# Optimization experiments

Measured on AMD Instinct MI355X. Metric: run time of the kernel, lower is better.

Reference implementation:

```python
import jax, jax.numpy as jnp
import numpy as np

B, C, RES, WS, HEADS, GROUPS, MLP_DIM = 16, 256, 56, 7, 8, 16, 1024
HEAD_DIM = C // HEADS
N = WS * WS  # tokens per window


def _rel_index(ws):
    coords = np.stack(np.meshgrid(np.arange(ws), np.arange(ws), indexing='ij'), 0).reshape(2, -1)
    rel = (coords[:, :, None] - coords[:, None, :]).transpose(1, 2, 0) + ws - 1
    return jnp.asarray(rel[..., 0] * (2 * ws - 1) + rel[..., 1], jnp.int32)


def setup_inputs() -> dict:
    key = jax.random.key(0)
    ks = jax.random.split(key, 8)
    s = 0.02
    return {
        'x': jax.random.normal(ks[0], (B, C, RES, RES), jnp.float32),
        'qkv_w': jax.random.normal(ks[1], (3 * C, C), jnp.float32) * s,
        'qkv_b': jnp.zeros((3 * C,), jnp.float32),
        'logit_scale': jnp.full((HEADS,), np.log(10.0), jnp.float32),
        'bias_table': jax.random.normal(ks[2], ((2 * WS - 1) ** 2, HEADS), jnp.float32) * s,
        'rel_index': _rel_index(WS),
        'proj_w': jax.random.normal(ks[3], (C, C), jnp.float32) * s,
        'proj_b': jnp.zeros((C,), jnp.float32),
        'gn1_w': jnp.ones((C,), jnp.float32), 'gn1_b': jnp.zeros((C,), jnp.float32),
        'gn2_w': jnp.ones((C,), jnp.float32), 'gn2_b': jnp.zeros((C,), jnp.float32),
        'mlp_gn_w': jnp.ones((C,), jnp.float32), 'mlp_gn_b': jnp.zeros((C,), jnp.float32),
        'mlp_w1': jax.random.normal(ks[4], (MLP_DIM, C), jnp.float32) * s,
        'mlp_b1': jnp.zeros((MLP_DIM,), jnp.float32),
        'mlp_w2': jax.random.normal(ks[5], (C, MLP_DIM), jnp.float32) * s,
        'mlp_b2': jnp.zeros((C,), jnp.float32),
    }


def _group_norm(x, w, b, groups, eps=1e-5):
    bn, c, h, ww = x.shape
    xg = x.reshape(bn, groups, c // groups, h, ww)
    m = xg.mean((2, 3, 4), keepdims=True)
    v = xg.var((2, 3, 4), keepdims=True)
    xg = (xg - m) * jax.lax.rsqrt(v + eps)
    return xg.reshape(bn, c, h, ww) * w[None, :, None, None] + b[None, :, None, None]


def _window_cosine_attn(x, qkv_w, qkv_b, logit_scale, bias_table, rel_index, proj_w, proj_b):
    bn, c, hh, ww = x.shape
    nh, nw = hh // WS, ww // WS
    # partition into non-overlapping WSxWS windows -> [bn*nh*nw, N, C]
    xw = x.reshape(bn, c, nh, WS, nw, WS).transpose(0, 2, 4, 3, 5, 1).reshape(bn * nh * nw, N, c)
    qkv = xw @ qkv_w.T + qkv_b
    qkv = qkv.reshape(-1, N, 3, HEADS, HEAD_DIM).transpose(2, 0, 3, 1, 4)
    q, k, v = qkv[0], qkv[1], qkv[2]  # [Bw, heads, N, d]
    # cosine attention (Swin v2): l2-normalized q/k, learnable clamped logit scale
    qn = q / jnp.clip(jnp.linalg.norm(q, axis=-1, keepdims=True), 1e-12)
    kn = k / jnp.clip(jnp.linalg.norm(k, axis=-1, keepdims=True), 1e-12)
    scale = jnp.exp(jnp.minimum(logit_scale, jnp.log(100.0)))[None, :, None, None]
    attn = jnp.einsum('bhnd,bhmd->bhnm', qn, kn) * scale
    bias = bias_table[rel_index].transpose(2, 0, 1)  # [heads, N, N]
    attn = jax.nn.softmax(attn + bias[None], axis=-1)
    out = jnp.einsum('bhnm,bhmd->bhnd', attn, v)
    out = out.transpose(0, 2, 1, 3).reshape(-1, N, c) @ proj_w.T + proj_b
    # reverse window partition -> [bn, c, H, W]
    out = out.reshape(bn, nh, nw, WS, WS, c).transpose(0, 5, 1, 3, 2, 4).reshape(bn, c, hh, ww)
    return out


def reference(x, qkv_w, qkv_b, logit_scale, bias_table, rel_index, proj_w, proj_b,
              gn1_w, gn1_b, gn2_w, gn2_b, mlp_gn_w, mlp_gn_b, mlp_w1, mlp_b1, mlp_w2, mlp_b2):
    h = _window_cosine_attn(x, qkv_w, qkv_b, logit_scale, bias_table, rel_index, proj_w, proj_b)
    h = jax.nn.relu(_group_norm(x + h, gn1_w, gn1_b, GROUPS))
    # ConvMLP: GroupNorm -> 1x1 conv -> act -> 1x1 conv
    m = _group_norm(h, mlp_gn_w, mlp_gn_b, GROUPS)
    m = jax.nn.relu(jnp.einsum('bchw,ec->behw', m, mlp_w1) + mlp_b1[None, :, None, None])
    m = jnp.einsum('behw,ce->bchw', m, mlp_w2) + mlp_b2[None, :, None, None]
    z = jax.nn.relu(_group_norm(h + m, gn2_w, gn2_b, GROUPS))
    return z
```

## Files before the change

kernel.cpp:

```cpp
#include <hip/hip_runtime.h>
#include <hip/hip_bf16.h>

typedef unsigned short u16;
typedef u16 u16x8 __attribute__((ext_vector_type(8)));
typedef u16 u16x4 __attribute__((ext_vector_type(4)));
typedef __bf16 bf16x8 __attribute__((ext_vector_type(8)));
typedef float f32x4 __attribute__((ext_vector_type(4)));

#define B_      16
#define C_      256
#define RES_    56
#define HW_     3136
#define NTOK    49
#define HEADS_  8
#define HD_     32
#define GROUPS_ 16
#define MLPD    1024
#define M_TOT   50176

__device__ __forceinline__ float b2f(u16 u){
  unsigned int x = ((unsigned int)u) << 16;
  return __builtin_bit_cast(float, x);
}
__device__ __forceinline__ u16 f2b(float f){
  __hip_bfloat16 h = __float2bfloat16(f);
  return __builtin_bit_cast(u16, h);
}
__device__ __forceinline__ bool sniff_f32(const void* sniff){
  return ((const u16*)sniff)[0] != (u16)0x3F80;
}
__device__ __forceinline__ float ldf(const void* p, size_t i, bool f32){
  return f32 ? ((const float*)p)[i] : b2f(((const u16*)p)[i]);
}
__device__ __forceinline__ void load8(const void* p, size_t off, bool f32, float* v){
  if (f32){
    const float* s = (const float*)p + off;
    float4 a = *(const float4*)s, b = *(const float4*)(s + 4);
    v[0]=a.x; v[1]=a.y; v[2]=a.z; v[3]=a.w; v[4]=b.x; v[5]=b.y; v[6]=b.z; v[7]=b.w;
  } else {
    u16x8 u = *(const u16x8*)((const u16*)p + off);
    #pragma unroll
    for (int j=0;j<8;++j) v[j] = b2f(u[j]);
  }
}

__device__ __forceinline__ void gload16(const u16* g, u16* l){
  __builtin_amdgcn_global_load_lds(
      (const __attribute__((address_space(1))) unsigned int*)g,
      (__attribute__((address_space(3))) unsigned int*)l, 16, 0, 0);
}

__device__ __forceinline__ int tok_of(int base_hw, int i){
  int ic = i < 48 ? i : 48;
  int q = (ic*37) >> 8;
  return base_hw + q*RES_ + (ic - q*7);
}

enum { M_QKV=0, M_PROJ=1, M_MLP1=2, M_MLP2=3 };

template<int MODE>
__global__ __launch_bounds__(256)
void mgemm(const u16* __restrict__ A, const u16* __restrict__ Bseg,
           const void* __restrict__ bias, void* __restrict__ Cp,
           const void* __restrict__ resid, const void* __restrict__ sniff)
{
  constexpr int KK = (MODE==M_MLP2) ? 1024 : 256;
  const int nx  = gridDim.x;
  const int bid = blockIdx.y * nx + blockIdx.x;
  const int cpx = (nx * gridDim.y) >> 3;
  const int swz = (bid & 7) * cpx + (bid >> 3);
  const int n0 = (swz % nx) * 128;
  const int m0 = (swz / nx) * 128;

  __shared__ alignas(16) u16 As[128*64];
  __shared__ alignas(16) u16 Bs[128*64];
  const int tid  = threadIdx.x;
  const int lane = tid & 63, w = tid >> 6;
  const int wm = w >> 1, wn = w & 1;
  const int lr = lane & 15, lk = lane >> 4;

  const int grow = lane >> 3, gcolg = (lane & 7) ^ (lane >> 3);
  size_t aoff[4], boff[4];
  #pragma unroll
  for (int i=0;i<4;++i){
    const int row = w*32 + i*8 + grow;
    aoff[i] = (size_t)(m0 + row)*KK + gcolg*8;
    boff[i] = (size_t)(n0 + row)*KK + gcolg*8;
  }

  f32x4 acc[4][4];
  #pragma unroll
  for (int i=0;i<4;++i)
    #pragma unroll
    for (int j=0;j<4;++j) acc[i][j] = (f32x4){0.f,0.f,0.f,0.f};

  for (int k0 = 0; k0 < KK; k0 += 64){
    if (k0) __syncthreads();
    #pragma unroll
    for (int i=0;i<4;++i){
      gload16(A    + aoff[i] + k0, As + (w*4+i)*512);
      gload16(Bseg + boff[i] + k0, Bs + (w*4+i)*512);
    }
    __syncthreads();
    #pragma unroll
    for (int kh=0; kh<2; ++kh){
      bf16x8 af[4], bfr[4];
      #pragma unroll
      for (int mf=0;mf<4;++mf){
        int row = wm*64 + mf*16 + lr;
        int idx = (row*64 + (kh*4 + lk)*8) ^ ((row&7)*8);
        af[mf] = *(const bf16x8*)(As + idx);
      }
      #pragma unroll
      for (int nf=0;nf<4;++nf){
        int row = wn*64 + nf*16 + lr;
        int idx = (row*64 + (kh*4 + lk)*8) ^ ((row&7)*8);
        bfr[nf] = *(const bf16x8*)(Bs + idx);
      }
      #pragma unroll
      for (int mf=0;mf<4;++mf)
        #pragma unroll
        for (int nf=0;nf<4;++nf)
          acc[mf][nf] = __builtin_amdgcn_mfma_f32_16x16x32_bf16(af[mf], bfr[nf], acc[mf][nf], 0,0,0);
    }
  }

  const bool f32 = sniff_f32(sniff);
  float bv[4];
  #pragma unroll
  for (int nf=0;nf<4;++nf) bv[nf] = ldf(bias, (size_t)(n0 + wn*64 + nf*16 + lr), f32);

  #pragma unroll
  for (int mf=0;mf<4;++mf){
    #pragma unroll
    for (int r=0;r<4;++r){
      const int row = m0 + wm*64 + mf*16 + lk*4 + r;
      #pragma unroll
      for (int nf=0;nf<4;++nf){
        const int col = n0 + wn*64 + nf*16 + lr;
        float v = acc[mf][nf][r] + bv[nf];
        if (MODE == M_QKV){
          ((u16*)Cp)[(size_t)row*768 + col] = f2b(v);
        } else if (MODE == M_PROJ){
          v += b2f(((const u16*)resid)[(size_t)row*C_ + col]);
          ((float*)Cp)[(size_t)row*C_ + col] = v;
        } else if (MODE == M_MLP1){
          ((u16*)Cp)[(size_t)row*MLPD + col] = f2b(fmaxf(v, 0.f));
        } else {
          v += ((const float*)resid)[(size_t)row*C_ + col];
          ((float*)Cp)[(size_t)row*C_ + col] = v;
        }
      }
    }
  }
}

__global__ __launch_bounds__(256)
void xt_kernel(const void* __restrict__ x, u16* __restrict__ xbf,
               const void* __restrict__ sniff){
  const bool f32 = sniff_f32(sniff);
  const int hw0 = blockIdx.x*64, c0 = blockIdx.y*64, b = blockIdx.z;
  __shared__ float tile[64][65];
  const int t = threadIdx.x;
  {
    int r = t >> 2, p = t & 3;
    size_t src = ((size_t)(b*C_ + c0 + r))*HW_ + hw0 + p*16;
    float v[16];
    load8(x, src, f32, v);
    load8(x, src + 8, f32, v + 8);
    #pragma unroll
    for (int e=0;e<16;++e) tile[p*16+e][r] = v[e];
  }
  __syncthreads();
  {
    int r2 = t >> 2, p2 = t & 3;
    u16x8 o0, o1;
    #pragma unroll
    for (int e=0;e<8;++e){ o0[e] = f2b(tile[r2][p2*16+e]); o1[e] = f2b(tile[r2][p2*16+8+e]); }
    size_t dst = ((size_t)(b*HW_ + hw0 + r2))*C_ + c0 + p2*16;
    *(u16x8*)(xbf + dst)     = o0;
    *(u16x8*)(xbf + dst + 8) = o1;
  }
}

__global__ __launch_bounds__(256)
void wconv(const void* __restrict__ src, u16* __restrict__ dst, int n,
           const void* __restrict__ sniff){
  const bool f32 = sniff_f32(sniff);
  int i = (blockIdx.x*256 + threadIdx.x)*8;
  if (i >= n) return;
  float v[8];
  load8(src, (size_t)i, f32, v);
  u16x8 u;
  #pragma unroll
  for (int j=0;j<8;++j) u[j] = f2b(v[j]);
  *(u16x8*)(dst + i) = u;
}

__global__ __launch_bounds__(256)
void bias_pre(const void* __restrict__ bias_table, const int* __restrict__ rel_index,
              float* __restrict__ out, float* __restrict__ rmax,
              const void* __restrict__ sniff){
  const bool f32 = sniff_f32(sniff);
  int h = blockIdx.x;
  for (int idx = threadIdx.x; idx < NTOK*NTOK; idx += 256)
    out[h*NTOK*NTOK + idx] = ldf(bias_table, (size_t)rel_index[idx]*HEADS_ + h, f32);
  __syncthreads();
  for (int i = threadIdx.x; i < NTOK; i += 256){
    const float* row = out + (h*NTOK + i)*NTOK;
    float m = row[0];
    for (int j=1;j<NTOK;++j) m = fmaxf(m, row[j]);
    rmax[h*NTOK + i] = m;
  }
}

__global__ __launch_bounds__(256)
void attn_kernel(const u16* __restrict__ qkv, u16* __restrict__ attnout,
                 const void* __restrict__ logit_scale, const float* __restrict__ biasD,
                 const float* __restrict__ biasRM, const void* __restrict__ sniff)
{
  const bool f32 = sniff_f32(sniff);
  const int h = blockIdx.x & 7, w = blockIdx.x >> 3;
  const int b = w >> 6, wr = (w >> 3) & 7, wc = w & 7;
  const int tid = threadIdx.x;
  const int wv = tid >> 6, lane = tid & 63;
  const int lr = lane & 15, lg = lane >> 4;
  const int base_hw = (wr*7)*RES_ + wc*7;
  const size_t qbase = (size_t)b*HW_*768;

  __shared__ alignas(16) u16 Qn[64][40];
  __shared__ alignas(16) u16 Kn[64][40];
  __shared__ alignas(16) u16 Vt[32][72];
  __shared__ alignas(16) u16 Pl[64][72];

  const float scale = __expf(fminf(ldf(logit_scale, h, f32), 4.6051701860f));

  if (wv == 0){
    u16 vrow[32];
    if (lane < NTOK){
      const u16* src = qkv + qbase + (size_t)tok_of(base_hw, lane)*768 + 512 + h*HD_;
      u16x8 a0 = *(const u16x8*)(src), a1 = *(const u16x8*)(src+8);
      u16x8 a2 = *(const u16x8*)(src+16), a3 = *(const u16x8*)(src+24);
      #pragma unroll
      for (int e=0;e<8;++e){ vrow[e]=a0[e]; vrow[8+e]=a1[e]; vrow[16+e]=a2[e]; vrow[24+e]=a3[e]; }
    } else {
      #pragma unroll
      for (int e=0;e<32;++e) vrow[e] = 0;
    }
    #pragma unroll
    for (int d=0;d<32;++d) Vt[d][lane] = vrow[d];
  } else if (wv == 1 || wv == 2){
    float fv[32];
    if (lane < NTOK){
      const u16* src = qkv + qbase + (size_t)tok_of(base_hw, lane)*768
                     + (wv == 2 ? 0 : 256) + h*HD_;
      #pragma unroll
      for (int c8=0;c8<4;++c8){
        u16x8 u = *(const u16x8*)(src + c8*8);
        #pragma unroll
        for (int e=0;e<8;++e) fv[c8*8+e] = b2f(u[e]);
      }
    } else {
      #pragma unroll
      for (int e=0;e<32;++e) fv[e] = 0.f;
    }
    float ss = 0.f;
    #pragma unroll
    for (int d=0;d<32;++d) ss += fv[d]*fv[d];
    float inv = (wv == 2 ? scale : 1.f) / fmaxf(sqrtf(ss), 1e-12f);
    u16* dst = (wv == 2) ? &Qn[lane][0] : &Kn[lane][0];
    #pragma unroll
    for (int c8=0;c8<4;++c8){
      u16x8 u;
      #pragma unroll
      for (int e=0;e<8;++e) u[e] = f2b(fv[c8*8+e]*inv);
      *(u16x8*)(dst + c8*8) = u;
    }
  }
  __syncthreads();

  const int mt = wv;
  const int i0 = mt*16;

  bf16x8 af = *(const bf16x8*)&Qn[i0 + lr][lg*8];
  f32x4 s[4];
  #pragma unroll
  for (int nt=0;nt<4;++nt){
    bf16x8 bq = *(const bf16x8*)&Kn[nt*16 + lr][lg*8];
    f32x4 c;
    #pragma unroll
    for (int r=0;r<4;++r){
      int i = i0 + lg*4 + r; if (i > 48) i = 48;
      int j = nt*16 + lr;    if (j > 48) j = 48;
      c[r] = biasD[((size_t)h*NTOK + i)*NTOK + j];
    }
    s[nt] = __builtin_amdgcn_mfma_f32_16x16x32_bf16(af, bq, c, 0,0,0);
  }

  float isum[4];
  #pragma unroll
  for (int r=0;r<4;++r){
    const int i = i0 + lg*4 + r;
    const int ic = i > 48 ? 48 : i;
    const float m = scale + biasRM[h*NTOK + ic];
    float ps = 0.f;
    #pragma unroll
    for (int nt=0;nt<4;++nt){
      const int j = nt*16 + lr;
      float p = (j < NTOK) ? __expf(s[nt][r] - m) : 0.f;
      Pl[i][j] = f2b(p);
      ps += p;
    }
    ps += __shfl_xor(ps,1); ps += __shfl_xor(ps,2);
    ps += __shfl_xor(ps,4); ps += __shfl_xor(ps,8);
    isum[r] = 1.f / ps;
  }

  f32x4 o[2];
  o[0] = (f32x4){0.f,0.f,0.f,0.f};
  o[1] = (f32x4){0.f,0.f,0.f,0.f};
  #pragma unroll
  for (int kk=0;kk<2;++kk){
    bf16x8 pa = *(const bf16x8*)&Pl[i0 + lr][kk*32 + lg*8];
    #pragma unroll
    for (int nt=0;nt<2;++nt){
      bf16x8 pb = *(const bf16x8*)&Vt[nt*16 + lr][kk*32 + lg*8];
      o[nt] = __builtin_amdgcn_mfma_f32_16x16x32_bf16(pa, pb, o[nt], 0,0,0);
    }
  }

  #pragma unroll
  for (int r=0;r<4;++r){
    const int i = i0 + lg*4 + r;
    if (i < NTOK){
      size_t ob = ((size_t)(b*HW_) + tok_of(base_hw, i))*C_ + h*HD_;
      attnout[ob + lr]      = f2b(o[0][r] * isum[r]);
      attnout[ob + 16 + lr] = f2b(o[1][r] * isum[r]);
    }
  }
}

__global__ __launch_bounds__(256)
void stats_part(const float* __restrict__ buf, float2* __restrict__ part){
  int chunk = blockIdx.x & 7;
  int g = (blockIdx.x >> 3) & 15;
  int b = blockIdx.x >> 7;
  const float* base = buf + (size_t)b*HW_*C_ + (size_t)chunk*392*C_ + g*16;
  float s=0.f, q=0.f;
  for (int i4 = threadIdx.x; i4 < 392*4; i4 += 256){
    const float4 v = *(const float4*)(base + (size_t)(i4>>2)*C_ + (i4&3)*4);
    s += v.x+v.y+v.z+v.w;
    q += v.x*v.x + v.y*v.y + v.z*v.z + v.w*v.w;
  }
  #pragma unroll
  for (int o=32;o>0;o>>=1){ s += __shfl_down(s,o); q += __shfl_down(q,o); }
  __shared__ float rs[4], rq[4];
  int wv = threadIdx.x >> 6;
  if ((threadIdx.x & 63) == 0){ rs[wv]=s; rq[wv]=q; }
  __syncthreads();
  if (threadIdx.x == 0)
    part[blockIdx.x] = make_float2(rs[0]+rs[1]+rs[2]+rs[3], rq[0]+rq[1]+rq[2]+rq[3]);
}

__global__ __launch_bounds__(256)
void stats_fin(const float2* __restrict__ part, float2* __restrict__ st,
               float2* __restrict__ AB, const void* __restrict__ w,
               const void* __restrict__ bb, const void* __restrict__ sniff){
  int t = threadIdx.x;
  float s=0.f, q=0.f;
  #pragma unroll
  for (int c=0;c<8;++c){ float2 p = part[t*8+c]; s += p.x; q += p.y; }
  float mean = s * (1.f/50176.f);
  float var  = fmaxf(q * (1.f/50176.f) - mean*mean, 0.f);
  float rsig = rsqrtf(var + 1e-5f);
  st[t] = make_float2(mean, rsig);
  if (AB){
    const bool f32 = sniff_f32(sniff);
    int b = t >> 4, g = t & 15;
    #pragma unroll
    for (int e=0;e<16;++e){
      int k = g*16 + e;
      float a = rsig * ldf(w, k, f32);
      AB[b*256 + k] = make_float2(a, ldf(bb, k, f32) - mean*a);
    }
  }
}

__global__ __launch_bounds__(256)
void stats_fin2(const float2* __restrict__ part2, float2* __restrict__ st,
                float2* __restrict__ AB, const void* __restrict__ w,
                const void* __restrict__ bb, const void* __restrict__ sniff){
  int t = threadIdx.x;
  int b = t >> 4, g = t & 15;
  float s=0.f, q=0.f;
  for (int i=0;i<392;++i){
    float2 p = part2[(size_t)(b*392 + i)*16 + g];
    s += p.x; q += p.y;
  }
  float mean = s * (1.f/50176.f);
  float var  = fmaxf(q * (1.f/50176.f) - mean*mean, 0.f);
  float rsig = rsqrtf(var + 1e-5f);
  st[t] = make_float2(mean, rsig);
  const bool f32 = sniff_f32(sniff);
  #pragma unroll
  for (int e=0;e<16;++e){
    int k = g*16 + e;
    float a = rsig * ldf(w, k, f32);
    AB[b*256 + k] = make_float2(a, ldf(bb, k, f32) - mean*a);
  }
}

__global__ __launch_bounds__(256)
void gnrelu_kernel(const float* __restrict__ Y, const float2* __restrict__ AB1,
                   float2* __restrict__ part2, float* __restrict__ H){
  size_t base = (size_t)blockIdx.x * 2048;
  int b = blockIdx.x / 392;
  int t = threadIdx.x;
  int off = t * 8;
  int c0 = off & 255;
  const float* src = Y + base + off;
  float4 a0 = *(const float4*)src, a1 = *(const float4*)(src+4);
  float tv[8] = {a0.x,a0.y,a0.z,a0.w,a1.x,a1.y,a1.z,a1.w};
  float o[8]; float s=0.f, q=0.f;
  #pragma unroll
  for (int j=0;j<8;++j){
    float2 ab = AB1[b*256 + c0 + j];
    o[j] = fmaxf(tv[j]*ab.x + ab.y, 0.f);
    s += o[j]; q += o[j]*o[j];
  }
  float* dst = H + base + off;
  *(float4*)dst     = make_float4(o[0],o[1],o[2],o[3]);
  *(float4*)(dst+4) = make_float4(o[4],o[5],o[6],o[7]);
  __shared__ float Ls[256], Lq[256];
  Ls[t] = s; Lq[t] = q;
  __syncthreads();
  if (t < 16){
    float ss=0.f, qq=0.f;
    #pragma unroll
    for (int j=0;j<16;++j){
      int idx = t*2 + (j&1) + (j>>1)*32;
      ss += Ls[idx]; qq += Lq[idx];
    }
    part2[(size_t)blockIdx.x*16 + t] = make_float2(ss,qq);
  }
}

__global__ __launch_bounds__(256)
void hnorm_kernel(const float* __restrict__ H, const float2* __restrict__ AB,
                  u16* __restrict__ Hn){
  size_t base = (size_t)blockIdx.x * 2048;
  int b = blockIdx.x / 392;
  int off = threadIdx.x * 8;
  int c0 = off & 255;
  const float* src = H + base + off;
  float4 a0 = *(const float4*)src, a1 = *(const float4*)(src+4);
  float t[8] = {a0.x,a0.y,a0.z,a0.w,a1.x,a1.y,a1.z,a1.w};
  u16x8 u;
  #pragma unroll
  for (int j=0;j<8;++j){
    float2 ab = AB[b*256 + c0 + j];
    u[j] = f2b(t[j]*ab.x + ab.y);
  }
  *(u16x8*)(Hn + base + off) = u;
}

__global__ __launch_bounds__(256)
void out_kernel(const float* __restrict__ T, const float2* __restrict__ AB2,
                void* __restrict__ outp, const void* __restrict__ sniff){
  const bool f32 = sniff_f32(sniff);
  int hw0 = blockIdx.x*64, c0 = blockIdx.y*64, b = blockIdx.z;
  __shared__ float tile[64][68];
  {
    int r = threadIdx.x >> 2, p = threadIdx.x & 3;
    const float* src = T + ((size_t)(b*HW_ + hw0 + r))*C_ + c0 + p*16;
    #pragma unroll
    for (int q4=0; q4<4; ++q4){
      float4 vv = *(const float4*)(src + q4*4);
      float tv[4] = {vv.x,vv.y,vv.z,vv.w};
      #pragma unroll
      for (int e=0;e<4;++e){
        int cl = p*16 + q4*4 + e;
        int c = c0 + cl;
        float2 ab = AB2[b*256 + c];
        tile[cl][r] = fmaxf(tv[e]*ab.x + ab.y, 0.f);
      }
    }
  }
  __syncthreads();
  {
    int r2 = threadIdx.x >> 2, p2 = threadIdx.x & 3;
    size_t ob = ((size_t)(b*C_ + c0 + r2))*HW_ + hw0 + p2*16;
    if (f32){
      float* op = (float*)outp;
      #pragma unroll
      for (int q4=0;q4<4;++q4){
        float4 vv = *(const float4*)&tile[r2][p2*16 + q4*4];
        *(float4*)(op + ob + q4*4) = vv;
      }
    } else {
      u16* op = (u16*)outp;
      u16x8 u0, u1;
      #pragma unroll
      for (int e=0;e<8;++e) u0[e] = f2b(tile[r2][p2*16 + e]);
      #pragma unroll
      for (int e=0;e<8;++e) u1[e] = f2b(tile[r2][p2*16 + 8 + e]);
      *(u16x8*)(op + ob)     = u0;
      *(u16x8*)(op + ob + 8) = u1;
    }
  }
}

__global__ void marker_kernel(u16* o){ o[threadIdx.x] = 0x4640; }

extern "C" void kernel_launch(void* const* d_in, const int* in_sizes, int n_in,
                              void* d_out, int out_size, void* d_ws, size_t ws_size,
                              hipStream_t stream)
{
  const void* x           = d_in[0];
  const void* qkv_w       = d_in[1];
  const void* qkv_b       = d_in[2];
  const void* logit_scale = d_in[3];
  const void* bias_table  = d_in[4];
  const int*  rel_index   = (const int*)d_in[5];
  const void* proj_w      = d_in[6];
  const void* proj_b      = d_in[7];
  const void* gn1_w       = d_in[8];
  const void* gn1_b       = d_in[9];
  const void* gn2_w       = d_in[10];
  const void* gn2_b       = d_in[11];
  const void* mgn_w       = d_in[12];
  const void* mgn_b       = d_in[13];
  const void* w1          = d_in[14];
  const void* b1          = d_in[15];
  const void* w2          = d_in[16];
  const void* b2          = d_in[17];

  char* ws = (char*)d_ws;
  const size_t o_qkv  = 0ull;
  const size_t o_attn = 77070336ull;
  const size_t o_Y    = 102760448ull;
  const size_t o_H    = 154140672ull;
  const size_t o_st   = 205520896ull;
  const size_t o_wbf  = 205527040ull;
  const size_t o_bd   = 207099904ull;
  const size_t o_brm  = 207176736ull;
  const size_t o_ab   = 207178304ull;
  const size_t o_pt   = 207211072ull;
  const size_t o_ab1  = 207227456ull;
  const size_t o_ab2  = 207260224ull;
  const size_t o_p2   = 207292992ull;
  const size_t need   = 208095808ull;
  if (ws_size < need){
    marker_kernel<<<1, 256, 0, stream>>>((u16*)d_out);
    return;
  }

  u16*   qkvbuf  = (u16*)(ws + o_qkv);
  u16*   attnbuf = (u16*)(ws + o_attn);
  float* Y       = (float*)(ws + o_Y);
  float* H       = (float*)(ws + o_H);
  u16*   xbf     = (u16*)(ws + o_H);
  u16*   Hn      = (u16*)(ws + o_Y);
  u16*   M1      = (u16*)(ws + o_qkv);
  float* T       = (float*)(ws + o_Y);
  float2* st1    = (float2*)(ws + o_st);
  float2* stm    = st1 + 256;
  float2* st2    = stm + 256;
  u16*   wq      = (u16*)(ws + o_wbf);
  u16*   wp      = wq + 768*256;
  u16*   w1b     = wp + 256*256;
  u16*   w2b     = w1b + 1024*256;
  float* biasD   = (float*)(ws + o_bd);
  float* biasRM  = (float*)(ws + o_brm);
  float2* ABm    = (float2*)(ws + o_ab);
  float2* parts  = (float2*)(ws + o_pt);
  float2* AB1    = (float2*)(ws + o_ab1);
  float2* AB2    = (float2*)(ws + o_ab2);
  float2* part2  = (float2*)(ws + o_p2);
  const void* sniff = gn1_w;

  wconv        <<<  96, 256, 0, stream>>>(qkv_w,  wq,  768*256,  sniff);
  wconv        <<<  32, 256, 0, stream>>>(proj_w, wp,  256*256,  sniff);
  wconv        <<< 128, 256, 0, stream>>>(w1,     w1b, 1024*256, sniff);
  wconv        <<< 128, 256, 0, stream>>>(w2,     w2b, 256*1024, sniff);
  bias_pre     <<<   8, 256, 0, stream>>>(bias_table, rel_index, biasD, biasRM, sniff);
  xt_kernel    <<<dim3(49,4,16), 256, 0, stream>>>(x, xbf, sniff);

  mgemm<M_QKV ><<<dim3(6,392), 256, 0, stream>>>(xbf, wq, qkv_b, qkvbuf, nullptr, sniff);
  attn_kernel  <<<8192, 256, 0, stream>>>(qkvbuf, attnbuf, logit_scale, biasD, biasRM, sniff);
  mgemm<M_PROJ><<<dim3(2,392), 256, 0, stream>>>(attnbuf, wp, proj_b, Y, xbf, sniff);
  stats_part   <<<2048, 256, 0, stream>>>(Y, parts);
  stats_fin    <<<1, 256, 0, stream>>>(parts, st1, AB1, gn1_w, gn1_b, sniff);
  gnrelu_kernel<<<6272, 256, 0, stream>>>(Y, AB1, part2, H);
  stats_fin2   <<<1, 256, 0, stream>>>(part2, stm, ABm, mgn_w, mgn_b, sniff);
  hnorm_kernel <<<6272, 256, 0, stream>>>(H, ABm, Hn);
  mgemm<M_MLP1><<<dim3(8,392), 256, 0, stream>>>(Hn, w1b, b1, M1, nullptr, sniff);
  mgemm<M_MLP2><<<dim3(2,392), 256, 0, stream>>>(M1, w2b, b2, T, H, sniff);
  stats_part   <<<2048, 256, 0, stream>>>(T, parts);
  stats_fin    <<<1, 256, 0, stream>>>(parts, st2, AB2, gn2_w, gn2_b, sniff);
  out_kernel   <<<dim3(49,4,16), 256, 0, stream>>>(T, AB2, d_out, sniff);
}
```

Before: 325.9 us.

## Fuse GroupNorm statistics into GEMM epilogues and store H as bf16

The PROJ and MLP2 GEMM epilogues now accumulate per-group sums and sums of squares, split at batch boundaries, and write per-tile partials. This removes the two full-tensor stats_part passes. A new finalize kernel runs over 16 blocks and the finalize step is parallelised per batch. The intermediate H is stored as bf16 instead of fp32, cutting traffic in hnorm and in the MLP2 residual read. The risk is lower precision in the residual path, plus extra shuffle reductions and a block barrier in the GEMM epilogue.

```diff
diff --git a/kernel.cpp b/kernel.cpp
--- a/kernel.cpp
+++ b/kernel.cpp
@@ -62,9 +62,11 @@
 __global__ __launch_bounds__(256)
 void mgemm(const u16* __restrict__ A, const u16* __restrict__ Bseg,
            const void* __restrict__ bias, void* __restrict__ Cp,
-           const void* __restrict__ resid, const void* __restrict__ sniff)
+           const void* __restrict__ resid, float2* __restrict__ partE,
+           const void* __restrict__ sniff)
 {
   constexpr int KK = (MODE==M_MLP2) ? 1024 : 256;
+  constexpr bool STATS = (MODE==M_PROJ || MODE==M_MLP2);
   const int nx  = gridDim.x;
   const int bid = blockIdx.y * nx + blockIdx.x;
   const int cpx = (nx * gridDim.y) >> 3;
@@ -74,6 +76,7 @@
 
   __shared__ alignas(16) u16 As[128*64];
   __shared__ alignas(16) u16 Bs[128*64];
+  __shared__ float pS[4][2][4], pQ[4][2][4];
   const int tid  = threadIdx.x;
   const int lane = tid & 63, w = tid >> 6;
   const int wm = w >> 1, wn = w & 1;
@@ -130,6 +133,11 @@
   #pragma unroll
   for (int nf=0;nf<4;++nf) bv[nf] = ldf(bias, (size_t)(n0 + wn*64 + nf*16 + lr), f32);
 
+  const int b0 = m0 / HW_;
+  const int splitB = (b0+1)*HW_;
+  float sv[2][4] = {{0.f,0.f,0.f,0.f},{0.f,0.f,0.f,0.f}};
+  float qv[2][4] = {{0.f,0.f,0.f,0.f},{0.f,0.f,0.f,0.f}};
+
   #pragma unroll
   for (int mf=0;mf<4;++mf){
     #pragma unroll
@@ -141,16 +149,36 @@
         float v = acc[mf][nf][r] + bv[nf];
         if (MODE == M_QKV){
           ((u16*)Cp)[(size_t)row*768 + col] = f2b(v);
-        } else if (MODE == M_PROJ){
-          v += b2f(((const u16*)resid)[(size_t)row*C_ + col]);
-          ((float*)Cp)[(size_t)row*C_ + col] = v;
         } else if (MODE == M_MLP1){
           ((u16*)Cp)[(size_t)row*MLPD + col] = f2b(fmaxf(v, 0.f));
         } else {
-          v += ((const float*)resid)[(size_t)row*C_ + col];
+          v += b2f(((const u16*)resid)[(size_t)row*C_ + col]);
           ((float*)Cp)[(size_t)row*C_ + col] = v;
+          if constexpr (STATS){
+            int slot = row >= splitB ? 1 : 0;
+            sv[slot][nf] += v; qv[slot][nf] += v*v;
+          }
         }
       }
+    }
+  }
+
+  if constexpr (STATS){
+    #pragma unroll
+    for (int sl=0;sl<2;++sl)
+      #pragma unroll
+      for (int nf=0;nf<4;++nf){
+        float s = sv[sl][nf], q = qv[sl][nf];
+        #pragma unroll
+        for (int m=1;m<64;m<<=1){ s += __shfl_xor(s,m); q += __shfl_xor(q,m); }
+        if (lane == 0){ pS[w][sl][nf] = s; pQ[w][sl][nf] = q; }
+      }
+    __syncthreads();
+    if (tid < 16){
+      int slot = tid >> 3, gi = tid & 7, wn_ = gi >> 2, nf = gi & 3;
+      float s = pS[wn_][slot][nf] + pS[2+wn_][slot][nf];
+      float q = pQ[wn_][slot][nf] + pQ[2+wn_][slot][nf];
+      partE[(((size_t)((m0>>7)*2 + (n0>>7)))*2 + slot)*8 + gi] = make_float2(s,q);
     }
   }
 }
@@ -341,45 +369,33 @@
 }
 
 __global__ __launch_bounds__(256)
-void stats_part(const float* __restrict__ buf, float2* __restrict__ part){
-  int chunk = blockIdx.x & 7;
-  int g = (blockIdx.x >> 3) & 15;
-  int b = blockIdx.x >> 7;
-  const float* base = buf + (size_t)b*HW_*C_ + (size_t)chunk*392*C_ + g*16;
-  float s=0.f, q=0.f;
-  for (int i4 = threadIdx.x; i4 < 392*4; i4 += 256){
-    const float4 v = *(const float4*)(base + (size_t)(i4>>2)*C_ + (i4&3)*4);
-    s += v.x+v.y+v.z+v.w;
-    q += v.x*v.x + v.y*v.y + v.z*v.z + v.w*v.w;
-  }
-  #pragma unroll
-  for (int o=32;o>0;o>>=1){ s += __shfl_down(s,o); q += __shfl_down(q,o); }
-  __shared__ float rs[4], rq[4];
-  int wv = threadIdx.x >> 6;
-  if ((threadIdx.x & 63) == 0){ rs[wv]=s; rq[wv]=q; }
+void statsE_fin(const float2* __restrict__ partE, float2* __restrict__ AB,
+                const void* __restrict__ w, const void* __restrict__ bb,
+                const void* __restrict__ sniff){
+  const int b = blockIdx.x, t = threadIdx.x;
+  const int g = t & 15, ch = t >> 4;
+  const int ntI = g >> 3, gi = g & 7;
+  float s = 0.f, q = 0.f;
+  int mt0 = ch*25, mt1 = mt0 + 25 > 392 ? 392 : mt0 + 25;
+  for (int mt = mt0; mt < mt1; ++mt){
+    int b0 = (mt*128)/HW_;
+    size_t base = ((size_t)(mt*2 + ntI))*16;
+    if (b0 == b)    { float2 p = partE[base + gi];     s += p.x; q += p.y; }
+    if (b0 + 1 == b){ float2 p = partE[base + 8 + gi]; s += p.x; q += p.y; }
+  }
+  __shared__ float Ls[256], Lq[256];
+  Ls[t] = s; Lq[t] = q;
   __syncthreads();
-  if (threadIdx.x == 0)
-    part[blockIdx.x] = make_float2(rs[0]+rs[1]+rs[2]+rs[3], rq[0]+rq[1]+rq[2]+rq[3]);
-}
-
-__global__ __launch_bounds__(256)
-void stats_fin(const float2* __restrict__ part, float2* __restrict__ st,
-               float2* __restrict__ AB, const void* __restrict__ w,
-               const void* __restrict__ bb, const void* __restrict__ sniff){
-  int t = threadIdx.x;
-  float s=0.f, q=0.f;
-  #pragma unroll
-  for (int c=0;c<8;++c){ float2 p = part[t*8+c]; s += p.x; q += p.y; }
-  float mean = s * (1.f/50176.f);
-  float var  = fmaxf(q * (1.f/50176.f) - mean*mean, 0.f);
-  float rsig = rsqrtf(var + 1e-5f);
-  st[t] = make_float2(mean, rsig);
-  if (AB){
+  if (t < 16){
+    float ss = 0.f, qq = 0.f;
+    #pragma unroll
+    for (int c=0;c<16;++c){ ss += Ls[c*16 + t]; qq += Lq[c*16 + t]; }
+    float mean = ss * (1.f/50176.f);
+    float var  = fmaxf(qq * (1.f/50176.f) - mean*mean, 0.f);
+    float rsig = rsqrtf(var + 1e-5f);
     const bool f32 = sniff_f32(sniff);
-    int b = t >> 4, g = t & 15;
-    #pragma unroll
     for (int e=0;e<16;++e){
-      int k = g*16 + e;
+      int k = t*16 + e;
       float a = rsig * ldf(w, k, f32);
       AB[b*256 + k] = make_float2(a, ldf(bb, k, f32) - mean*a);
     }
@@ -387,32 +403,39 @@
 }
 
 __global__ __launch_bounds__(256)
-void stats_fin2(const float2* __restrict__ part2, float2* __restrict__ st,
-                float2* __restrict__ AB, const void* __restrict__ w,
-                const void* __restrict__ bb, const void* __restrict__ sniff){
-  int t = threadIdx.x;
-  int b = t >> 4, g = t & 15;
-  float s=0.f, q=0.f;
-  for (int i=0;i<392;++i){
+void stats_fin2(const float2* __restrict__ part2, float2* __restrict__ AB,
+                const void* __restrict__ w, const void* __restrict__ bb,
+                const void* __restrict__ sniff){
+  const int b = blockIdx.x, t = threadIdx.x;
+  const int g = t & 15, ch = t >> 4;
+  float s = 0.f, q = 0.f;
+  int i0 = ch*25, i1 = i0 + 25 > 392 ? 392 : i0 + 25;
+  for (int i = i0; i < i1; ++i){
     float2 p = part2[(size_t)(b*392 + i)*16 + g];
     s += p.x; q += p.y;
   }
-  float mean = s * (1.f/50176.f);
-  float var  = fmaxf(q * (1.f/50176.f) - mean*mean, 0.f);
-  float rsig = rsqrtf(var + 1e-5f);
-  st[t] = make_float2(mean, rsig);
-  const bool f32 = sniff_f32(sniff);
-  #pragma unroll
-  for (int e=0;e<16;++e){
-    int k = g*16 + e;
-    float a = rsig * ldf(w, k, f32);
-    AB[b*256 + k] = make_float2(a, ldf(bb, k, f32) - mean*a);
+  __shared__ float Ls[256], Lq[256];
+  Ls[t] = s; Lq[t] = q;
+  __syncthreads();
+  if (t < 16){
+    float ss = 0.f, qq = 0.f;
+    #pragma unroll
+    for (int c=0;c<16;++c){ ss += Ls[c*16 + t]; qq += Lq[c*16 + t]; }
+    float mean = ss * (1.f/50176.f);
+    float var  = fmaxf(qq * (1.f/50176.f) - mean*mean, 0.f);
+    float rsig = rsqrtf(var + 1e-5f);
+    const bool f32 = sniff_f32(sniff);
+    for (int e=0;e<16;++e){
+      int k = t*16 + e;
+      float a = rsig * ldf(w, k, f32);
+      AB[b*256 + k] = make_float2(a, ldf(bb, k, f32) - mean*a);
+    }
   }
 }
 
 __global__ __launch_bounds__(256)
 void gnrelu_kernel(const float* __restrict__ Y, const float2* __restrict__ AB1,
-                   float2* __restrict__ part2, float* __restrict__ H){
+                   float2* __restrict__ part2, u16* __restrict__ Hb){
   size_t base = (size_t)blockIdx.x * 2048;
   int b = blockIdx.x / 392;
   int t = threadIdx.x;
@@ -421,16 +444,15 @@
   const float* src = Y + base + off;
   float4 a0 = *(const float4*)src, a1 = *(const float4*)(src+4);
   float tv[8] = {a0.x,a0.y,a0.z,a0.w,a1.x,a1.y,a1.z,a1.w};
-  float o[8]; float s=0.f, q=0.f;
+  u16x8 u; float s=0.f, q=0.f;
   #pragma unroll
   for (int j=0;j<8;++j){
     float2 ab = AB1[b*256 + c0 + j];
-    o[j] = fmaxf(tv[j]*ab.x + ab.y, 0.f);
-    s += o[j]; q += o[j]*o[j];
-  }
-  float* dst = H + base + off;
-  *(float4*)dst     = make_float4(o[0],o[1],o[2],o[3]);
-  *(float4*)(dst+4) = make_float4(o[4],o[5],o[6],o[7]);
+    float o = fmaxf(tv[j]*ab.x + ab.y, 0.f);
+    u[j] = f2b(o);
+    s += o; q += o*o;
+  }
+  *(u16x8*)(Hb + base + off) = u;
   __shared__ float Ls[256], Lq[256];
   Ls[t] = s; Lq[t] = q;
   __syncthreads();
@@ -446,20 +468,18 @@
 }
 
 __global__ __launch_bounds__(256)
-void hnorm_kernel(const float* __restrict__ H, const float2* __restrict__ AB,
+void hnorm_kernel(const u16* __restrict__ Hb, const float2* __restrict__ AB,
                   u16* __restrict__ Hn){
   size_t base = (size_t)blockIdx.x * 2048;
   int b = blockIdx.x / 392;
   int off = threadIdx.x * 8;
   int c0 = off & 255;
-  const float* src = H + base + off;
-  float4 a0 = *(const float4*)src, a1 = *(const float4*)(src+4);
-  float t[8] = {a0.x,a0.y,a0.z,a0.w,a1.x,a1.y,a1.z,a1.w};
+  u16x8 uin = *(const u16x8*)(Hb + base + off);
   u16x8 u;
   #pragma unroll
   for (int j=0;j<8;++j){
     float2 ab = AB[b*256 + c0 + j];
-    u[j] = f2b(t[j]*ab.x + ab.y);
+    u[j] = f2b(b2f(uin[j])*ab.x + ab.y);
   }
   *(u16x8*)(Hn + base + off) = u;
 }
@@ -545,7 +565,6 @@
   const size_t o_bd   = 207099904ull;
   const size_t o_brm  = 207176736ull;
   const size_t o_ab   = 207178304ull;
-  const size_t o_pt   = 207211072ull;
   const size_t o_ab1  = 207227456ull;
   const size_t o_ab2  = 207260224ull;
   const size_t o_p2   = 207292992ull;
@@ -558,14 +577,11 @@
   u16*   qkvbuf  = (u16*)(ws + o_qkv);
   u16*   attnbuf = (u16*)(ws + o_attn);
   float* Y       = (float*)(ws + o_Y);
-  float* H       = (float*)(ws + o_H);
+  u16*   Hb      = (u16*)(ws + o_H);
   u16*   xbf     = (u16*)(ws + o_H);
   u16*   Hn      = (u16*)(ws + o_Y);
   u16*   M1      = (u16*)(ws + o_qkv);
   float* T       = (float*)(ws + o_Y);
-  float2* st1    = (float2*)(ws + o_st);
-  float2* stm    = st1 + 256;
-  float2* st2    = stm + 256;
   u16*   wq      = (u16*)(ws + o_wbf);
   u16*   wp      = wq + 768*256;
   u16*   w1b     = wp + 256*256;
@@ -573,10 +589,10 @@
   float* biasD   = (float*)(ws + o_bd);
   float* biasRM  = (float*)(ws + o_brm);
   float2* ABm    = (float2*)(ws + o_ab);
-  float2* parts  = (float2*)(ws + o_pt);
   float2* AB1    = (float2*)(ws + o_ab1);
   float2* AB2    = (float2*)(ws + o_ab2);
   float2* part2  = (float2*)(ws + o_p2);
+  float2* partE  = (float2*)(ws + o_p2);
   const void* sniff = gn1_w;
 
   wconv        <<<  96, 256, 0, stream>>>(qkv_w,  wq,  768*256,  sniff);
@@ -586,17 +602,15 @@
   bias_pre     <<<   8, 256, 0, stream>>>(bias_table, rel_index, biasD, biasRM, sniff);
   xt_kernel    <<<dim3(49,4,16), 256, 0, stream>>>(x, xbf, sniff);
 
-  mgemm<M_QKV ><<<dim3(6,392), 256, 0, stream>>>(xbf, wq, qkv_b, qkvbuf, nullptr, sniff);
+  mgemm<M_QKV ><<<dim3(6,392), 256, 0, stream>>>(xbf, wq, qkv_b, qkvbuf, nullptr, nullptr, sniff);
   attn_kernel  <<<8192, 256, 0, stream>>>(qkvbuf, attnbuf, logit_scale, biasD, biasRM, sniff);
-  mgemm<M_PROJ><<<dim3(2,392), 256, 0, stream>>>(attnbuf, wp, proj_b, Y, xbf, sniff);
-  stats_part   <<<2048, 256, 0, stream>>>(Y, parts);
-  stats_fin    <<<1, 256, 0, stream>>>(parts, st1, AB1, gn1_w, gn1_b, sniff);
-  gnrelu_kernel<<<6272, 256, 0, stream>>>(Y, AB1, part2, H);
-  stats_fin2   <<<1, 256, 0, stream>>>(part2, stm, ABm, mgn_w, mgn_b, sniff);
-  hnorm_kernel <<<6272, 256, 0, stream>>>(H, ABm, Hn);
-  mgemm<M_MLP1><<<dim3(8,392), 256, 0, stream>>>(Hn, w1b, b1, M1, nullptr, sniff);
-  mgemm<M_MLP2><<<dim3(2,392), 256, 0, stream>>>(M1, w2b, b2, T, H, sniff);
-  stats_part   <<<2048, 256, 0, stream>>>(T, parts);
-  stats_fin    <<<1, 256, 0, stream>>>(parts, st2, AB2, gn2_w, gn2_b, sniff);
+  mgemm<M_PROJ><<<dim3(2,392), 256, 0, stream>>>(attnbuf, wp, proj_b, Y, xbf, partE, sniff);
+  statsE_fin   <<<16, 256, 0, stream>>>(partE, AB1, gn1_w, gn1_b, sniff);
+  gnrelu_kernel<<<6272, 256, 0, stream>>>(Y, AB1, part2, Hb);
+  stats_fin2   <<<16, 256, 0, stream>>>(part2, ABm, mgn_w, mgn_b, sniff);
+  hnorm_kernel <<<6272, 256, 0, stream>>>(Hb, ABm, Hn);
+  mgemm<M_MLP1><<<dim3(8,392), 256, 0, stream>>>(Hn, w1b, b1, M1, nullptr, nullptr, sniff);
+  mgemm<M_MLP2><<<dim3(2,392), 256, 0, stream>>>(M1, w2b, b2, T, Hb, partE, sniff);
+  statsE_fin   <<<16, 256, 0, stream>>>(partE, AB2, gn2_w, gn2_b, sniff);
   out_kernel   <<<dim3(49,4,16), 256, 0, stream>>>(T, AB2, d_out, sniff);
 }
```

Result: faster. 313.1 us (-3.9%).
